# Kernel optimization log

Hardware: AMD Instinct MI355X
Metric: run time of the kernel (lower is better)

The kernel has to match this reference:

```python
import jax, jax.numpy as jnp
import numpy as np

H = W = 96                      # image_size (scaled down from (240,240) for working-set control)
K = 16                          # faces_per_pixel
SIGMA = 1e-4
GAMMA = 1e-4
BLUR = float(np.log(1.0 / 1e-4 - 1.0) * SIGMA)   # blur_radius, compared against squared NDC dist (pytorch3d convention)
ZNEAR, ZFAR = 1.0, 100.0        # softmax_rgb_blend defaults
EPS = 1e-10


def _edge_d2(p, a, b):
    # squared point-to-segment distance; p:[B,P,F,2], a,b:[B,1,F,2]
    ab = b - a
    ap = p - a
    t = jnp.clip((ap * ab).sum(-1) / ((ab * ab).sum(-1) + 1e-12), 0.0, 1.0)
    d = ap - t[..., None] * ab
    return (d * d).sum(-1)


def _render(meshes_positions, meshes_rotations, meshes_scale, cam_pos, cam_rot, vertices, vert_colors, faces_packed):
    B, M, _ = meshes_positions.shape
    V = vertices.shape[1]
    # per-mesh scale -> rotate -> translate (forward of MeshesRenderer)
    scaled = meshes_scale[:, :, None, :] * vertices[None]                           # [B,M,V,3]
    world = jnp.einsum('bmij,bmvj->bmvi', meshes_rotations, scaled) + meshes_positions[:, :, None, :]
    world = world.reshape(B, M * V, 3)
    # pytorch3d camera: X_cam = X_world @ R + T
    cam = jnp.einsum('bvj,bji->bvi', world, cam_rot) + cam_pos[:, None, :]
    z = cam[..., 2]                                                                 # [B,N]
    xy = cam[..., :2] / z[..., None]                                                # perspective, focal=1 (NDC)

    tri = xy[:, faces_packed]                                                       # [B,F,3,2]
    tz = z[:, faces_packed]                                                         # [B,F,3]
    fcol = vert_colors.reshape(M * V, 3)[faces_packed]                              # [F,3,3]

    xs = (jnp.arange(W, dtype=xy.dtype) + 0.5) * 2.0 / W - 1.0
    ys = 1.0 - (jnp.arange(H, dtype=xy.dtype) + 0.5) * 2.0 / H
    gx, gy = jnp.meshgrid(xs, ys)
    pix = jnp.stack([gx.ravel(), gy.ravel()], -1)[None, :, None, :]                 # [1,P,1,2]

    v0 = tri[:, None, :, 0]; v1 = tri[:, None, :, 1]; v2 = tri[:, None, :, 2]       # [B,1,F,2]
    e1 = v1 - v0; e2 = v2 - v0
    d = pix - v0                                                                    # [B,P,F,2]
    den = e1[..., 0] * e2[..., 1] - e1[..., 1] * e2[..., 0] + 1e-12
    b1 = (d[..., 0] * e2[..., 1] - d[..., 1] * e2[..., 0]) / den                    # barycentrics [B,P,F]
    b2 = (e1[..., 0] * d[..., 1] - e1[..., 1] * d[..., 0]) / den
    b0 = 1.0 - b1 - b2
    zpix = b0 * tz[:, None, :, 0] + b1 * tz[:, None, :, 1] + b2 * tz[:, None, :, 2]
    inside = (b0 >= 0) & (b1 >= 0) & (b2 >= 0)
    d2 = jnp.minimum(jnp.minimum(_edge_d2(pix, v0, v1), _edge_d2(pix, v1, v2)), _edge_d2(pix, v2, v0))
    dists = jnp.where(inside, -d2, d2)                                              # signed squared dist
    valid = (zpix > 1e-2) & (dists <= BLUR)

    # faces_per_pixel = K nearest faces by depth (z-buffer)
    _, idx = jax.lax.top_k(jnp.where(valid, -zpix, -jnp.inf), K)                    # [B,P,K]
    take = lambda a: jnp.take_along_axis(a, idx, axis=-1)
    bk = jnp.stack([take(b0), take(b1), take(b2)], -1)                              # [B,P,K,3]
    zk, dk = take(zpix), take(dists)
    mk = take(valid.astype(zpix.dtype))
    # texture gather: barycentric blend of per-vertex colors (TexturesVertex.sample_textures)
    texel = jnp.einsum('bpkv,bpkvc->bpkc', bk, fcol[idx])                           # [B,P,K,3]

    # softmax_rgb_blend
    prob = jax.nn.sigmoid(-dk / SIGMA) * mk
    zinv = (ZFAR - zk) / (ZFAR - ZNEAR) * mk
    zmax = jnp.maximum(zinv.max(-1), EPS)
    wnum = prob * jnp.exp((zinv - zmax[..., None]) / GAMMA)
    delta = jnp.exp((EPS - zmax) / GAMMA)
    denom = wnum.sum(-1) + delta
    bg = jnp.ones(3, zpix.dtype)                                                    # default white background
    rgb = ((wnum[..., None] * texel).sum(-2) + delta[..., None] * bg) / denom[..., None]
    alpha = 1.0 - jnp.prod(1.0 - prob, -1)
    return jnp.concatenate([rgb, alpha[..., None]], -1).reshape(B, H, W, 4)


def setup_inputs() -> dict:
    key = jax.random.key(0)
    ks = jax.random.split(key, 8)
    B, M, V, Fm = 2, 2, 256, 256
    vertices = jax.random.normal(ks[0], (M, V, 3), jnp.float32) * 0.4
    faces = jax.random.randint(ks[1], (M, Fm, 3), 0, V)
    vert_colors = jax.random.uniform(ks[2], (M, V, 3), dtype=jnp.float32)
    meshes_positions = jax.random.normal(ks[3], (B, M, 3), jnp.float32) * 0.2
    # small z-axis rotations (proper rotation matrices)
    ang = jax.random.normal(ks[4], (B, M), jnp.float32) * 0.2
    c, s = jnp.cos(ang), jnp.sin(ang)
    z0 = jnp.zeros_like(c); o = jnp.ones_like(c)
    meshes_rotations = jnp.stack([c, -s, z0, s, c, z0, z0, z0, o], -1).reshape(B, M, 3, 3)
    meshes_scale = 1.0 + 0.1 * jax.random.normal(ks[5], (B, M, 3), jnp.float32)
    cam_rot = jnp.tile(jnp.eye(3, dtype=jnp.float32)[None], (B, 1, 1))
    cam_pos = jnp.tile(jnp.array([0.0, 0.0, 3.0], jnp.float32), (B, 1))
    return {
        'meshes_positions': meshes_positions, 'meshes_rotations': meshes_rotations,
        'meshes_scale': meshes_scale, 'cam_pos': cam_pos, 'cam_rot': cam_rot,
        'vertices': vertices, 'faces': faces, 'vert_colors': vert_colors,
    }


def reference(meshes_positions, meshes_rotations, meshes_scale, cam_pos, cam_rot, vertices, faces, vert_colors):
    M, V = vertices.shape[:2]
    faces_packed = (faces + (jnp.arange(M) * V)[:, None, None]).reshape(-1, 3)      # [F,3]
    return _render(meshes_positions, meshes_rotations, meshes_scale, cam_pos, cam_rot,
                   vertices, vert_colors, faces_packed)
```

## Files before the change

kernel.cpp:

```cpp
#include <hip/hip_runtime.h>

#pragma clang fp contract(off)

#define HH 96
#define WW 96
#define KK 16
#define MM 2
#define NF 512
#define NV 512
#define NPIX (HH*WW)
#define TDIM 12
#define TSZ 8
#define NTILE (TDIM*TDIM)
#define MAXC 8
#define BPT 8

#define SIGMA_F 1e-4f
#define GAMMA_F 1e-4f
#define BLUR_F  9.210240366975851e-4f
#define EPS_F   1e-10f
#define ZFAR_F  100.0f
#define ZNEAR_F 1.0f
#define RM      0.0304f

#define SENT 0xFFFFFFFFFFFFFFFFull

__device__ __forceinline__ float frcp(float x) { return __builtin_amdgcn_rcpf(x); }

__device__ __forceinline__ float edge_d2(float px, float py,
                                         float ax, float ay,
                                         float bx, float by) {
    float abx = bx - ax, aby = by - ay;
    float apx = px - ax, apy = py - ay;
    float t = (apx*abx + apy*aby) * frcp(abx*abx + aby*aby + 1e-12f);
    t = fminf(fmaxf(t, 0.0f), 1.0f);
    float dx = apx - t*abx, dy = apy - t*aby;
    return dx*dx + dy*dy;
}

struct Rast { float b0, b1, b2, zpix, dists; };

__device__ __forceinline__ Rast rasterize_s(float px, float py,
                                            float v0x, float v0y, float v1x, float v1y,
                                            float v2x, float v2y,
                                            float z0, float z1, float z2) {
    Rast r;
    float e1x=v1x-v0x, e1y=v1y-v0y, e2x=v2x-v0x, e2y=v2y-v0y;
    float dx=px-v0x, dy=py-v0y;
    float rden = frcp(e1x*e2y - e1y*e2x + 1e-12f);
    r.b1 = (dx*e2y - dy*e2x) * rden;
    r.b2 = (e1x*dy - e1y*dx) * rden;
    r.b0 = 1.0f - r.b1 - r.b2;
    r.zpix = r.b0*z0 + r.b1*z1 + r.b2*z2;
    bool inside = (r.b0 >= 0.0f) && (r.b1 >= 0.0f) && (r.b2 >= 0.0f);
    float d2 = edge_d2(px, py, v0x, v0y, v1x, v1y);
    d2 = fminf(d2, edge_d2(px, py, v1x, v1y, v2x, v2y));
    d2 = fminf(d2, edge_d2(px, py, v2x, v2y, v0x, v0y));
    r.dists = inside ? -d2 : d2;
    return r;
}

__device__ __forceinline__ unsigned long long packzf(float z, int id) {
    return (((unsigned long long)__float_as_uint(z)) << 32) | (unsigned int)id;
}

__device__ __forceinline__ unsigned long long shflx64(unsigned long long v, int m) {
    int lo = __shfl_xor((int)(unsigned)(v & 0xffffffffull), m, 64);
    int hi = __shfl_xor((int)(unsigned)(v >> 32), m, 64);
    return ((unsigned long long)(unsigned)hi << 32) | (unsigned)lo;
}

__device__ __forceinline__ int ring_tile(int ord) {
    int r = ((int)__builtin_sqrtf((float)ord)) >> 1;
    while ((2*r+2)*(2*r+2) <= ord) ++r;
    while (r > 0 && (2*r)*(2*r) > ord) --r;
    int p = ord - 4*r*r;
    int side = 2*r + 2;
    int lo = TDIM/2 - 1 - r;
    int hi = TDIM/2 + r;
    int tx, ty;
    if (p < side)              { ty = lo; tx = lo + p; }
    else if (p < 2*side - 1)   { tx = hi; ty = lo + (p - side + 1); }
    else if (p < 3*side - 2)   { ty = hi; tx = hi - (p - (2*side - 1) + 1); }
    else                       { tx = lo; ty = hi - (p - (3*side - 2) + 1); }
    return ty * TDIM + tx;
}

__global__ __launch_bounds__(512) void render_fused_kernel(
    const float* __restrict__ mpos,
    const float* __restrict__ mrot,
    const float* __restrict__ mscale,
    const float* __restrict__ cpos,
    const float* __restrict__ crot,
    const float* __restrict__ verts,
    const int*   __restrict__ faces,
    const float* __restrict__ vcol,
    float*       __restrict__ out)
{
    const int blocksPerB = NTILE * BPT;
    const int b    = blockIdx.x / blocksPerB;
    const int rem  = blockIdx.x % blocksPerB;
    const int tile = ring_tile(rem / BPT);
    const int q    = rem % BPT;
    const int wv   = threadIdx.x >> 6;
    const int lane = threadIdx.x & 63;
    const int t    = threadIdx.x;

    __shared__ float2 svxy[NV];
    __shared__ float  svz[NV];
    __shared__ float4 scol[NV];
    __shared__ float  sbx0[NF], sby0[NF], sbx1[NF], sby1[NF];
    __shared__ int    si0[NF], si1[NF], si2[NF];
    __shared__ int    cl0[NF], cl1[NF], cl2[NF];

    float cr[9];
    #pragma unroll
    for (int i = 0; i < 9; ++i) cr[i] = crot[b*9 + i];
    const float cpx = cpos[b*3+0], cpy = cpos[b*3+1], cpz = cpos[b*3+2];

    {
        int g = t;
        int m = g >> 8;
        int sb = (b*MM + m)*3, rb = (b*MM + m)*9;
        float v0 = verts[g*3+0] * mscale[sb+0];
        float v1 = verts[g*3+1] * mscale[sb+1];
        float v2 = verts[g*3+2] * mscale[sb+2];
        float wx = mrot[rb+0]*v0 + mrot[rb+1]*v1 + mrot[rb+2]*v2 + mpos[sb+0];
        float wy = mrot[rb+3]*v0 + mrot[rb+4]*v1 + mrot[rb+5]*v2 + mpos[sb+1];
        float wz = mrot[rb+6]*v0 + mrot[rb+7]*v1 + mrot[rb+8]*v2 + mpos[sb+2];
        float cx = wx*cr[0] + wy*cr[3] + wz*cr[6] + cpx;
        float cy = wx*cr[1] + wy*cr[4] + wz*cr[7] + cpy;
        float cz = wx*cr[2] + wy*cr[5] + wz*cr[8] + cpz;
        svxy[g] = make_float2(cx / cz, cy / cz);
        svz[g]  = cz;
        scol[g] = make_float4(vcol[g*3+0], vcol[g*3+1], vcol[g*3+2], 0.0f);
    }
    __syncthreads();

    {
        int f = t;
        int off = (f >> 8) << 8;
        int i0 = faces[f*3+0] + off;
        int i1 = faces[f*3+1] + off;
        int i2 = faces[f*3+2] + off;
        si0[f] = i0; si1[f] = i1; si2[f] = i2;
        float2 p0 = svxy[i0], p1 = svxy[i1], p2 = svxy[i2];
        sbx0[f] = fminf(fminf(p0.x,p1.x),p2.x);
        sby0[f] = fminf(fminf(p0.y,p1.y),p2.y);
        sbx1[f] = fmaxf(fmaxf(p0.x,p1.x),p2.x);
        sby1[f] = fmaxf(fmaxf(p0.y,p1.y),p2.y);
    }
    __syncthreads();

    const int ty = tile / TDIM, tx = tile % TDIM;
    const float x_lo = -1.0f + tx * (2.0f / TDIM);
    const float x_hi = x_lo + 2.0f / TDIM;
    const float y_hi = 1.0f - ty * (2.0f / TDIM);
    const float y_lo = y_hi - 2.0f / TDIM;

    float bx0[8], by0[8], bx1[8], by1[8];
    #pragma unroll
    for (int k = 0; k < 8; ++k) {
        int f = (k << 6) | lane;
        bx0[k] = sbx0[f]; by0[k] = sby0[f];
        bx1[k] = sbx1[f]; by1[k] = sby1[f];
    }
    int hitm = 0;
    #pragma unroll
    for (int k = 0; k < 8; ++k) {
        bool hit = (bx0[k] - RM <= x_hi) && (bx1[k] + RM >= x_lo) &&
                   (by0[k] - RM <= y_hi) && (by1[k] + RM >= y_lo);
        hitm |= (hit ? 1 : 0) << k;
    }
    int L = 0;
    #pragma unroll
    for (int k = 0; k < 8; ++k) {
        bool hit = (hitm >> k) & 1;
        unsigned long long m = __ballot(hit);
        if (hit) {
            int f = (k << 6) | lane;
            int pos = L + __popcll(m & ((1ull << lane) - 1ull));
            cl0[pos] = si0[f];
            cl1[pos] = si1[f];
            cl2[pos] = si2[f];
        }
        L += __popcll(m);
    }

    const int pi = ty * TSZ + q, pj = tx * TSZ + wv;
    const float px = ((float)pj + 0.5f) * (2.0f / WW) - 1.0f;
    const float py = 1.0f - ((float)pi + 0.5f) * (2.0f / HH);

    unsigned long long pk[MAXC];
    int validm = 0;
    #pragma unroll
    for (int c = 0; c < MAXC; ++c) {
        pk[c] = SENT;
        if (c * 64 < L) {
            int idx = c * 64 + lane;
            unsigned long long tt = SENT;
            if (idx < L) {
                int i0 = cl0[idx], i1 = cl1[idx], i2 = cl2[idx];
                float2 p0 = svxy[i0], p1 = svxy[i1], p2 = svxy[i2];
                float z0 = svz[i0], z1 = svz[i1], z2 = svz[i2];
                Rast r = rasterize_s(px, py, p0.x, p0.y, p1.x, p1.y,
                                     p2.x, p2.y, z0, z1, z2);
                if (r.zpix > 0.01f && r.dists <= BLUR_F) tt = packzf(r.zpix, idx);
            }
            pk[c] = tt;
            validm |= (tt != SENT ? 1 : 0) << c;
        }
    }

    const int c0 = __popc(validm);
    int cnt = c0;
    #pragma unroll
    for (int m = 1; m < 64; m <<= 1) cnt += __shfl_xor(cnt, m, 64);

    float nr = 0.0f, ng = 0.0f, nb = 0.0f, dn = 0.0f, ap = 1.0f;
    float zmaxv = EPS_F;

#define AGG(pp, zz) do { \
        int p_ = (pp); float z_ = (zz); \
        int i0_ = cl0[p_], i1_ = cl1[p_], i2_ = cl2[p_]; \
        float2 q0_ = svxy[i0_], q1_ = svxy[i1_], q2_ = svxy[i2_]; \
        float z0_ = svz[i0_], z1_ = svz[i1_], z2_ = svz[i2_]; \
        Rast r_ = rasterize_s(px, py, q0_.x, q0_.y, q1_.x, q1_.y, \
                              q2_.x, q2_.y, z0_, z1_, z2_); \
        float prob_ = frcp(1.0f + __expf(r_.dists / SIGMA_F)); \
        float zinv_ = (ZFAR_F - z_) / (ZFAR_F - ZNEAR_F); \
        float w_ = prob_ * __expf((zinv_ - zmaxv) / GAMMA_F); \
        float4 c0_ = scol[i0_], c1_ = scol[i1_], c2_ = scol[i2_]; \
        nr += w_ * (r_.b0*c0_.x + r_.b1*c1_.x + r_.b2*c2_.x); \
        ng += w_ * (r_.b0*c0_.y + r_.b1*c1_.y + r_.b2*c2_.y); \
        nb += w_ * (r_.b0*c0_.z + r_.b1*c1_.z + r_.b2*c2_.z); \
        dn += w_; \
        ap *= (1.0f - prob_); \
    } while (0)

    if (cnt <= KK) {
        unsigned long long lmin = pk[0];
        #pragma unroll
        for (int c = 1; c < MAXC; ++c) lmin = (pk[c] < lmin) ? pk[c] : lmin;
        #pragma unroll
        for (int m = 1; m < 64; m <<= 1) {
            unsigned long long o2 = shflx64(lmin, m);
            lmin = (o2 < lmin) ? o2 : lmin;
        }
        if (cnt > 0) {
            float zming = __uint_as_float((unsigned)(lmin >> 32));
            zmaxv = fmaxf((ZFAR_F - zming) / (ZFAR_F - ZNEAR_F), EPS_F);
        }
        #pragma unroll
        for (int c = 0; c < MAXC; ++c)
            if (validm & (1 << c)) {
                int id = (int)(pk[c] & 0xffffffffull);
                float z = __uint_as_float((unsigned)(pk[c] >> 32));
                AGG(id, z);
            }
    } else if (L <= 64) {
        unsigned long long v = pk[0];
        #pragma unroll
        for (int kk = 2; kk <= 64; kk <<= 1) {
            #pragma unroll
            for (int jj = kk >> 1; jj > 0; jj >>= 1) {
                unsigned long long o2 = shflx64(v, jj);
                bool kmin = ((lane & kk) == 0) == ((lane & jj) == 0);
                v = (kmin == (o2 < v)) ? o2 : v;
            }
        }
        unsigned z0b = (unsigned)__shfl((int)(unsigned)(v >> 32), 0, 64);
        zmaxv = fmaxf((ZFAR_F - __uint_as_float(z0b)) / (ZFAR_F - ZNEAR_F), EPS_F);
        if (lane < KK) {
            int id = (int)(v & 0xffffffffull);
            float z = __uint_as_float((unsigned)(v >> 32));
            AGG(id, z);
        }
    } else {
        int remm = validm, inclm = 0;
        float zming = 0.0f;
        for (int r = 0; r < KK; ++r) {
            unsigned long long lm = SENT;
            #pragma unroll
            for (int k = 0; k < MAXC; ++k)
                if (remm & (1 << k)) lm = (pk[k] < lm) ? pk[k] : lm;
            #pragma unroll
            for (int m = 1; m < 64; m <<= 1) {
                unsigned long long o2 = shflx64(lm, m);
                lm = (o2 < lm) ? o2 : lm;
            }
            if (r == 0) zming = __uint_as_float((unsigned)(lm >> 32));
            #pragma unroll
            for (int k = 0; k < MAXC; ++k)
                if ((remm & (1 << k)) && pk[k] == lm) { inclm |= 1 << k; remm &= ~(1 << k); }
        }
        zmaxv = fmaxf((ZFAR_F - zming) / (ZFAR_F - ZNEAR_F), EPS_F);
        #pragma unroll
        for (int k = 0; k < MAXC; ++k)
            if (inclm & (1 << k)) {
                int id = (int)(pk[k] & 0xffffffffull);
                float z = __uint_as_float((unsigned)(pk[k] >> 32));
                AGG(id, z);
            }
    }
#undef AGG

    #pragma unroll
    for (int m = 1; m < 64; m <<= 1) {
        nr += __shfl_xor(nr, m, 64);
        ng += __shfl_xor(ng, m, 64);
        nb += __shfl_xor(nb, m, 64);
        dn += __shfl_xor(dn, m, 64);
        ap *= __shfl_xor(ap, m, 64);
    }
    if (lane == 0) {
        float delta = __expf((EPS_F - zmaxv) / GAMMA_F);
        float dd = dn + delta;
        float4 o4;
        o4.x = (nr + delta) / dd;
        o4.y = (ng + delta) / dd;
        o4.z = (nb + delta) / dd;
        o4.w = 1.0f - ap;
        *reinterpret_cast<float4*>(&out[((size_t)b * NPIX + pi * WW + pj) * 4]) = o4;
    }
}

extern "C" void kernel_launch(void* const* d_in, const int* in_sizes, int n_in,
                              void* d_out, int out_size, void* d_ws, size_t ws_size,
                              hipStream_t stream) {
    const float* mpos   = (const float*)d_in[0];
    const float* mrot   = (const float*)d_in[1];
    const float* mscale = (const float*)d_in[2];
    const float* cpos   = (const float*)d_in[3];
    const float* crot   = (const float*)d_in[4];
    const float* verts  = (const float*)d_in[5];
    const int*   faces  = (const int*)d_in[6];
    const float* vcol   = (const float*)d_in[7];
    float*       out    = (float*)d_out;

    const int B = in_sizes[3] / 3;
    dim3 grid(B * NTILE * BPT), block(512);
    render_fused_kernel<<<grid, block, 0, stream>>>(
        mpos, mrot, mscale, cpos, crot, verts, faces, vcol, out);
}
```

Measured before the change: 39.19 us.

## Fuse blend accumulation into rasterization pass with online max rescaling

In the common case where a pixel has at most K candidate faces, the softmax blend is accumulated during the first rasterization pass using an online-softmax style running max per lane. A wave-wide max reduction and rescale then combine the lanes. This removes the second rasterization and the extra shared-memory loads for those pixels. The cost is extra exp and rescale work inside the candidate loop, which also runs for pixels that later take the sort paths, where the accumulators are reset and recomputed. A redundant exp call is left in the rescale branch.

```diff
diff --git a/kernel.cpp b/kernel.cpp
--- a/kernel.cpp
+++ b/kernel.cpp
@@ -193,6 +193,9 @@
 
     unsigned long long pk[MAXC];
     int validm = 0;
+    float nr = 0.0f, ng = 0.0f, nb = 0.0f, dn = 0.0f, ap = 1.0f;
+    float zm = EPS_F;
+
     #pragma unroll
     for (int c = 0; c < MAXC; ++c) {
         pk[c] = SENT;
@@ -205,7 +208,24 @@
                 float z0 = svz[i0], z1 = svz[i1], z2 = svz[i2];
                 Rast r = rasterize_s(px, py, p0.x, p0.y, p1.x, p1.y,
                                      p2.x, p2.y, z0, z1, z2);
-                if (r.zpix > 0.01f && r.dists <= BLUR_F) tt = packzf(r.zpix, idx);
+                if (r.zpix > 0.01f && r.dists <= BLUR_F) {
+                    tt = packzf(r.zpix, idx);
+                    float zinv = (ZFAR_F - r.zpix) / (ZFAR_F - ZNEAR_F);
+                    if (zinv > zm) {
+                        float s = __expf(zm - zinv);
+                        s = __expf((zm - zinv) / GAMMA_F);
+                        nr *= s; ng *= s; nb *= s; dn *= s;
+                        zm = zinv;
+                    }
+                    float prob = frcp(1.0f + __expf(r.dists / SIGMA_F));
+                    float w = prob * __expf((zinv - zm) / GAMMA_F);
+                    float4 c0_ = scol[i0], c1_ = scol[i1], c2_ = scol[i2];
+                    nr += w * (r.b0*c0_.x + r.b1*c1_.x + r.b2*c2_.x);
+                    ng += w * (r.b0*c0_.y + r.b1*c1_.y + r.b2*c2_.y);
+                    nb += w * (r.b0*c0_.z + r.b1*c1_.z + r.b2*c2_.z);
+                    dn += w;
+                    ap *= (1.0f - prob);
+                }
             }
             pk[c] = tt;
             validm |= (tt != SENT ? 1 : 0) << c;
@@ -217,8 +237,7 @@
     #pragma unroll
     for (int m = 1; m < 64; m <<= 1) cnt += __shfl_xor(cnt, m, 64);
 
-    float nr = 0.0f, ng = 0.0f, nb = 0.0f, dn = 0.0f, ap = 1.0f;
-    float zmaxv = EPS_F;
+    float zmaxv = zm;
 
 #define AGG(pp, zz) do { \
         int p_ = (pp); float z_ = (zz); \
@@ -239,26 +258,8 @@
     } while (0)
 
     if (cnt <= KK) {
-        unsigned long long lmin = pk[0];
-        #pragma unroll
-        for (int c = 1; c < MAXC; ++c) lmin = (pk[c] < lmin) ? pk[c] : lmin;
-        #pragma unroll
-        for (int m = 1; m < 64; m <<= 1) {
-            unsigned long long o2 = shflx64(lmin, m);
-            lmin = (o2 < lmin) ? o2 : lmin;
-        }
-        if (cnt > 0) {
-            float zming = __uint_as_float((unsigned)(lmin >> 32));
-            zmaxv = fmaxf((ZFAR_F - zming) / (ZFAR_F - ZNEAR_F), EPS_F);
-        }
-        #pragma unroll
-        for (int c = 0; c < MAXC; ++c)
-            if (validm & (1 << c)) {
-                int id = (int)(pk[c] & 0xffffffffull);
-                float z = __uint_as_float((unsigned)(pk[c] >> 32));
-                AGG(id, z);
-            }
     } else if (L <= 64) {
+        nr = 0.0f; ng = 0.0f; nb = 0.0f; dn = 0.0f; ap = 1.0f;
         unsigned long long v = pk[0];
         #pragma unroll
         for (int kk = 2; kk <= 64; kk <<= 1) {
@@ -277,6 +278,7 @@
             AGG(id, z);
         }
     } else {
+        nr = 0.0f; ng = 0.0f; nb = 0.0f; dn = 0.0f; ap = 1.0f;
         int remm = validm, inclm = 0;
         float zming = 0.0f;
         for (int r = 0; r < KK; ++r) {
@@ -306,6 +308,12 @@
 #undef AGG
 
     #pragma unroll
+    for (int m = 1; m < 64; m <<= 1) zmaxv = fmaxf(zmaxv, __shfl_xor(zmaxv, m, 64));
+    {
+        float s = __expf((zm - zmaxv) / GAMMA_F);
+        if (cnt <= KK) { nr *= s; ng *= s; nb *= s; dn *= s; }
+    }
+    #pragma unroll
     for (int m = 1; m < 64; m <<= 1) {
         nr += __shfl_xor(nr, m, 64);
         ng += __shfl_xor(ng, m, 64);
```

Measured after the change: 42.07 us. 1.07x slower.
